# Kernel tuning notes

Hardware: AMD Instinct MI355X
Metric: run time of the kernel (lower is better)

Reference implementation:

```python
import jax, jax.numpy as jnp
import numpy as np

MARGIN = 1.0
N, D, N_CLASSES = 8192, 256, 512


def setup_inputs() -> dict:
    key = jax.random.key(0)
    k1, k2 = jax.random.split(key)
    emb = jax.random.normal(k1, (N, D), dtype=jnp.float32)
    emb = emb / jnp.linalg.norm(emb, axis=1, keepdims=True)  # L2-normalized per docstring
    labels = jax.random.randint(k2, (N,), 0, N_CLASSES, dtype=jnp.int64)
    return {"embeddings": emb, "labels": labels}


def _pairwise_l2(x):
    # torch.cdist(x, x, p=2) via ||a||^2 + ||b||^2 - 2ab, with safe sqrt (zero grad at 0)
    sq = jnp.sum(x * x, axis=1)
    sqd = jnp.maximum(sq[:, None] + sq[None, :] - 2.0 * (x @ x.T), 0.0)
    pos = sqd > 0
    return jnp.where(pos, jnp.sqrt(jnp.where(pos, sqd, 1.0)), 0.0)


def _triplet_loss_semi_hard(embeddings, labels, margin):
    n = embeddings.shape[0]
    dist = _pairwise_l2(embeddings)                      # (N, N)
    labels_eq = labels[None, :] == labels[:, None]       # (N, N)
    labels_neq = ~labels_eq
    eye = jnp.eye(n, dtype=bool)
    pos_mask = labels_eq & ~eye
    valid_anchor = pos_mask.any(axis=1) & labels_neq.any(axis=1)

    NEG_INF = jnp.float32(-jnp.inf)
    POS_INF = jnp.float32(jnp.inf)
    # hardest positive per anchor (max dist among same-label, non-self)
    d_pos = jnp.max(jnp.where(pos_mask, dist, NEG_INF), axis=1)  # (N,)

    neg_dists_only = jnp.where(labels_neq, dist, POS_INF)
    # semi-hard: negatives with d_pos < d < d_pos + margin; fallback to hardest negative
    dp = d_pos[:, None]
    semi_mask = labels_neq & (dist > dp) & (dist < dp + margin)
    has_semi = semi_mask.any(axis=1)
    semi_idx = jnp.argmin(jnp.where(semi_mask, dist, POS_INF), axis=1)
    hard_idx = jnp.argmin(neg_dists_only, axis=1)
    neg_idx = jnp.where(has_semi, semi_idx, hard_idx)

    d_neg = jnp.take_along_axis(dist, neg_idx[:, None], axis=1)[:, 0]  # (N,)
    losses = jax.nn.relu(d_pos - d_neg + margin)
    valid_f = valid_anchor.astype(losses.dtype)
    # mean over valid anchors only (losses[valid_anchor].mean())
    return jnp.sum(losses * valid_f) / jnp.sum(valid_f)


def reference(embeddings, labels):
    return _triplet_loss_semi_hard(embeddings, labels, MARGIN)
```

## Files before the change

### kernel.cpp

```cpp
#include <hip/hip_runtime.h>
#include <hip/hip_bf16.h>
#include <math.h>

#define N 8192
#define D 256
#define MARGIN 1.0f

#define BM 128
#define BN 128
#define NCH 4
#define NB (N / BM)
#define NTRI (NB * (NB + 1) / 2)
#define NCONV (N * D / 4 / 256)
#define NCLS 512
#define CCAP 64
#define RPITCH 257

typedef __attribute__((ext_vector_type(8))) _Float16 half8;
typedef __attribute__((ext_vector_type(4))) _Float16 half4;
typedef __attribute__((ext_vector_type(4))) float f32x4;
typedef unsigned int uint32;
typedef unsigned long long u64;

__global__ __launch_bounds__(256) void k_prep(const float* __restrict__ x,
                                              const int* __restrict__ labels,
                                              _Float16* __restrict__ hp,
                                              float* __restrict__ dpos,
                                              u64* __restrict__ acc_pack,
                                              unsigned* __restrict__ counter) {
    const int b = blockIdx.x;
    const int t = threadIdx.x;

    if (b < NCONV) {
        int i = b * 256 + t;
        float4 v = reinterpret_cast<const float4*>(x)[i];
        half4 h;
        h[0] = (_Float16)v.x; h[1] = (_Float16)v.y;
        h[2] = (_Float16)v.z; h[3] = (_Float16)v.w;
        reinterpret_cast<half4*>(hp)[i] = h;
        if (b == 0 && t == 0) {
            *acc_pack = 0ull;
            *counter = 0u;
        }
        return;
    }

    __shared__ float rows[CCAP * RPITCH];
    __shared__ float sqv[CCAP];
    __shared__ int dpv[CCAP];
    __shared__ int mem[CCAP];
    __shared__ int nmem;

    const int c = b - NCONV;
    if (t == 0) nmem = 0;
    if (t < CCAP) dpv[t] = 0;
    __syncthreads();
    for (int base = 0; base < N; base += 256) {
        int j = base + t;
        if (labels[j] == c) {
            int p = atomicAdd(&nmem, 1);
            if (p < CCAP) mem[p] = j;
        }
    }
    __syncthreads();
    const int M = nmem < CCAP ? nmem : CCAP;

    for (int r = 0; r < M; ++r)
        rows[r * RPITCH + t] = x[(size_t)mem[r] * D + t];
    __syncthreads();

    if (t < M) {
        const float* rp = &rows[t * RPITCH];
        float s = 0.0f;
        for (int d = 0; d < D; ++d) s += rp[d] * rp[d];
        sqv[t] = s;
    }
    __syncthreads();

    for (int p = t; p < M * M; p += 256) {
        int i = p / M, j = p - i * M;
        const float* ri = &rows[i * RPITCH];
        const float* rj = &rows[j * RPITCH];
        float dot = 0.0f;
        for (int d = 0; d < D; ++d) dot = fmaf(ri[d], rj[d], dot);
        float sqd = fmaxf(sqv[i] + sqv[j] - 2.0f * dot, 0.0f);
        if (j != i) atomicMax(&dpv[i], __float_as_int(sqd));
    }
    __syncthreads();
    if (t < M)
        dpos[mem[t]] = (M > 1) ? sqrtf(__int_as_float(dpv[t])) : -1.0f;
}

__global__ __launch_bounds__(512) void k_main(const _Float16* __restrict__ hp,
                                              const int* __restrict__ labels,
                                              const float* __restrict__ dpos,
                                              float* __restrict__ pr_n,
                                              float* __restrict__ pr_s,
                                              float* __restrict__ pc_n,
                                              float* __restrict__ pc_s) {
    __shared__ char Abuf[2][BM * 128];
    __shared__ char Bbuf[2][BN * 128];
    __shared__ float rHi[BM], cHi[BN];
    __shared__ int rlab[BM], clab[BN];
    __shared__ float tmpn[4][BM], tmps[4][BM];

    const int t = threadIdx.x;
    int tb = blockIdx.x;
    int by = (int)((2 * NB + 1 - sqrtf((float)((2 * NB + 1) * (2 * NB + 1)) -
                                       8.0f * (float)tb)) * 0.5f);
    if (by < 0) by = 0;
    if (by > NB - 1) by = NB - 1;
    while (by > 0 && (by * NB - by * (by - 1) / 2) > tb) --by;
    while (((by + 1) * NB - (by + 1) * by / 2) <= tb) ++by;
    const int bx = by + (tb - (by * NB - by * (by - 1) / 2));
    const int r0 = by * BM, c0 = bx * BN;

    const int w = t >> 6, lane = t & 63;
    const int wr = w >> 2, wc = w & 3;

    if (t < BM) {
        rlab[t] = labels[r0 + t];
        float dp = dpos[r0 + t];
        rHi[t] = (2.0f - dp * dp) * 0.5f;
    } else if (t < 256) {
        int u = t - BM;
        clab[u] = labels[c0 + u];
        float dp = dpos[c0 + u];
        cHi[u] = (2.0f - dp * dp) * 0.5f;
    }

    f32x4 acc[4][2] = {};
    f32x4 accT[2][4] = {};

    const int srow = lane >> 3;
    const int scol = ((lane & 7) ^ srow) << 3;
    const _Float16* gA0 = hp + (size_t)(r0 + srow) * D + scol + (size_t)w * 8 * D;
    const _Float16* gB0 = hp + (size_t)(c0 + srow) * D + scol + (size_t)w * 8 * D;
    const int ldso = w * 1024 + lane * 16;

#define STAGE(bufA, bufB, k0e)                                                  \
    {                                                                           \
        _Pragma("unroll")                                                       \
        for (int q = 0; q < 2; ++q) {                                           \
            const _Float16* gpa = gA0 + q * (8 * 8 * D) + (k0e);                \
            const _Float16* gpb = gB0 + q * (8 * 8 * D) + (k0e);                \
            char* lpa = (bufA) + q * 8192 + ldso;                               \
            char* lpb = (bufB) + q * 8192 + ldso;                               \
            __builtin_amdgcn_global_load_lds(                                   \
                (__attribute__((address_space(1))) void*)(void*)gpa,            \
                (__attribute__((address_space(3))) void*)lpa, 16, 0, 0);        \
            __builtin_amdgcn_global_load_lds(                                   \
                (__attribute__((address_space(1))) void*)(void*)gpb,            \
                (__attribute__((address_space(3))) void*)lpb, 16, 0, 0);        \
        }                                                                       \
    }

    STAGE(Abuf[0], Bbuf[0], 0);
    asm volatile("s_waitcnt vmcnt(0)" ::: "memory");
    __syncthreads();

    const int g2 = lane >> 4;
    const int lr = lane & 15;
    const int rsw = lr & 7;

#pragma unroll 1
    for (int s = 0; s < NCH; ++s) {
        const int cur = s & 1;
        if (s < NCH - 1) STAGE(Abuf[cur ^ 1], Bbuf[cur ^ 1], (s + 1) * 64);

#pragma unroll
        for (int kk = 0; kk < 2; ++kk) {
            const int cb = kk * 64 + (g2 << 4);
            half8 aF[4], bF[2];
#pragma unroll
            for (int m = 0; m < 4; ++m) {
                int ra = wr * 64 + m * 16 + lr;
                aF[m] = *reinterpret_cast<const half8*>(
                    Abuf[cur] + ra * 128 + (cb ^ (rsw << 4)));
            }
#pragma unroll
            for (int n = 0; n < 2; ++n) {
                int rb = wc * 32 + n * 16 + lr;
                bF[n] = *reinterpret_cast<const half8*>(
                    Bbuf[cur] + rb * 128 + (cb ^ (rsw << 4)));
            }
#pragma unroll
            for (int m = 0; m < 4; ++m)
#pragma unroll
                for (int n = 0; n < 2; ++n)
                    acc[m][n] = __builtin_amdgcn_mfma_f32_16x16x32_f16(
                        aF[m], bF[n], acc[m][n], 0, 0, 0);
#pragma unroll
            for (int n = 0; n < 2; ++n)
#pragma unroll
                for (int m = 0; m < 4; ++m)
                    accT[n][m] = __builtin_amdgcn_mfma_f32_16x16x32_f16(
                        bF[n], aF[m], accT[n][m], 0, 0, 0);
        }
        __syncthreads();
    }
#undef STAGE

    const float NINF = -__builtin_inff();

    int rowm[4]; int rlm[4]; float rHim[4];
#pragma unroll
    for (int m = 0; m < 4; ++m) {
        rowm[m] = wr * 64 + m * 16 + lr;
        rlm[m] = rlab[rowm[m]];
        rHim[m] = rHi[rowm[m]];
    }
    int4 clA = *reinterpret_cast<const int4*>(&clab[wc * 32 + g2 * 4]);
    int4 clB = *reinterpret_cast<const int4*>(&clab[wc * 32 + 16 + g2 * 4]);
    const int clv[8] = {clA.x, clA.y, clA.z, clA.w, clB.x, clB.y, clB.z, clB.w};
    int coln[2]; int cln[2]; float cHin[2];
#pragma unroll
    for (int n = 0; n < 2; ++n) {
        coln[n] = wc * 32 + n * 16 + lr;
        cln[n] = clab[coln[n]];
        cHin[n] = cHi[coln[n]];
    }
    int rlq[16];
#pragma unroll
    for (int m = 0; m < 4; ++m) {
        int4 rv = *reinterpret_cast<const int4*>(&rlab[wr * 64 + m * 16 + g2 * 4]);
        rlq[m * 4 + 0] = rv.x; rlq[m * 4 + 1] = rv.y;
        rlq[m * 4 + 2] = rv.z; rlq[m * 4 + 3] = rv.w;
    }

#pragma unroll
    for (int m = 0; m < 4; ++m) {
        const int rl = rlm[m];
        const float aHi = rHim[m];
        float an = NINF, ag = NINF;
#pragma unroll
        for (int n = 0; n < 2; ++n)
#pragma unroll
            for (int reg = 0; reg < 4; ++reg) {
                float a = accT[n][m][reg];
                bool neq = (rl != clv[n * 4 + reg]);
                an = fmaxf(an, neq ? a : NINF);
                ag = fmaxf(ag, (neq && a < aHi) ? a : NINF);
            }
        an = fmaxf(an, __shfl_xor(an, 16, 64));
        an = fmaxf(an, __shfl_xor(an, 32, 64));
        ag = fmaxf(ag, __shfl_xor(ag, 16, 64));
        ag = fmaxf(ag, __shfl_xor(ag, 32, 64));
        if (g2 == 0) {
            tmpn[wc][rowm[m]] = an;
            tmps[wc][rowm[m]] = ag;
        }
    }
    __syncthreads();
    if (t < BM) {
        float a0 = fmaxf(tmpn[0][t], tmpn[1][t]);
        float a1 = fmaxf(tmpn[2][t], tmpn[3][t]);
        pr_n[(size_t)tb * BM + t] = fmaxf(a0, a1);
        float b0 = fmaxf(tmps[0][t], tmps[1][t]);
        float b1 = fmaxf(tmps[2][t], tmps[3][t]);
        pr_s[(size_t)tb * BM + t] = fmaxf(b0, b1);
    }
    __syncthreads();

#pragma unroll
    for (int n = 0; n < 2; ++n) {
        const int cl = cln[n];
        const float aHi = cHin[n];
        float an = NINF, ag = NINF;
#pragma unroll
        for (int m = 0; m < 4; ++m)
#pragma unroll
            for (int reg = 0; reg < 4; ++reg) {
                float a = acc[m][n][reg];
                bool neq = (cl != rlq[m * 4 + reg]);
                an = fmaxf(an, neq ? a : NINF);
                ag = fmaxf(ag, (neq && a < aHi) ? a : NINF);
            }
        an = fmaxf(an, __shfl_xor(an, 16, 64));
        an = fmaxf(an, __shfl_xor(an, 32, 64));
        ag = fmaxf(ag, __shfl_xor(ag, 16, 64));
        ag = fmaxf(ag, __shfl_xor(ag, 32, 64));
        if (lane < 16) {
            tmpn[wr][coln[n]] = an;
            tmps[wr][coln[n]] = ag;
        }
    }
    __syncthreads();
    if (t < BN) {
        pc_n[(size_t)tb * BN + t] = fmaxf(tmpn[0][t], tmpn[1][t]);
        pc_s[(size_t)tb * BN + t] = fmaxf(tmps[0][t], tmps[1][t]);
    }
}

__global__ __launch_bounds__(256) void k_finish(const float* __restrict__ dpos,
                                                const float* __restrict__ pr_n,
                                                const float* __restrict__ pr_s,
                                                const float* __restrict__ pc_n,
                                                const float* __restrict__ pc_s,
                                                u64* __restrict__ acc_pack,
                                                unsigned* __restrict__ counter,
                                                float* __restrict__ out) {
    __shared__ float shn[2][128], shs[2][128];
    __shared__ u64 wpart[2];
    const int q = blockIdx.x;
    const int t = threadIdx.x;
    const int half = t >> 7, a = t & 127;
    const int Lr = NB - q;
    const int base = q * NB - q * (q - 1) / 2;
    const int ntiles = Lr + q + 1;
    const float NINF = -__builtin_inff();

    float an = NINF, ag = NINF;
    for (int u = half; u < ntiles; u += 2) {
        size_t off;
        const float *Pn, *Ps;
        if (u < Lr) {
            off = (size_t)(base + u) * BM + a;
            Pn = pr_n; Ps = pr_s;
        } else {
            int byy = u - Lr;
            int tb2 = byy * NB - byy * (byy - 1) / 2 + (q - byy);
            off = (size_t)tb2 * BN + a;
            Pn = pc_n; Ps = pc_s;
        }
        an = fmaxf(an, Pn[off]);
        ag = fmaxf(ag, Ps[off]);
    }
    shn[half][a] = an;
    shs[half][a] = ag;
    __syncthreads();

    u64 pack = 0;
    if (t < 128) {
        an = fmaxf(shn[0][t], shn[1][t]);
        ag = fmaxf(shs[0][t], shs[1][t]);
        float dp = dpos[q * 128 + t];
        if (dp >= 0.0f && an > -1e37f) {
            float dphi = dp + MARGIN;
            float aLo = (2.0f - dphi * dphi) * 0.5f;
            float asel = (ag > aLo) ? ag : an;
            float fsq = fmaxf(fmaf(-2.0f, asel, 2.0f), 0.0f);
            float dn = sqrtf(fsq);
            float l = fmaxf(dp - dn + MARGIN, 0.0f);
            u64 lq = (u64)(l * 1073741824.0f + 0.5f);
            pack = (lq << 16) | 1ull;
        }
    }
    for (int m = 1; m <= 32; m <<= 1) pack += __shfl_xor(pack, m, 64);
    if (t < 128 && (t & 63) == 0) wpart[t >> 6] = pack;
    __syncthreads();
    if (t == 0) {
        atomicAdd(acc_pack, wpart[0] + wpart[1]);
        __threadfence();
        unsigned old = atomicAdd(counter, 1u);
        if (old == gridDim.x - 1) {
            u64 val = atomicAdd(acc_pack, (u64)0);
            double s = (double)(val >> 16) * (1.0 / 1073741824.0);
            double c = (double)(val & 0xFFFFull);
            out[0] = (float)(s / c);
        }
    }
}

extern "C" void kernel_launch(void* const* d_in, const int* in_sizes, int n_in,
                              void* d_out, int out_size, void* d_ws, size_t ws_size,
                              hipStream_t stream) {
    const float* x = (const float*)d_in[0];
    const int* labels = (const int*)d_in[1];
    float* out = (float*)d_out;

    u64* acc_pack = (u64*)d_ws;
    unsigned* counter = (unsigned*)(acc_pack + 1);
    float* dpos = (float*)(counter + 2);
    _Float16* hp = (_Float16*)(dpos + N);
    float* pr_n = (float*)(hp + (size_t)N * D);
    float* pr_s = pr_n + (size_t)NTRI * BM;
    float* pc_n = pr_s + (size_t)NTRI * BM;
    float* pc_s = pc_n + (size_t)NTRI * BM;

    hipLaunchKernelGGL(k_prep, dim3(NCONV + NCLS), dim3(256), 0, stream,
                       x, labels, hp, dpos, acc_pack, counter);
    hipLaunchKernelGGL(k_main, dim3(NTRI), dim3(512), 0, stream,
                       hp, labels, dpos, pr_n, pr_s, pc_n, pc_s);
    hipLaunchKernelGGL(k_finish, dim3(NB), dim3(256), 0, stream,
                       dpos, pr_n, pr_s, pc_n, pc_s, acc_pack, counter, out);
}
```

Before: 97.65 us.

## Fuse finish kernel into main kernel via trailing spin-wait blocks

Removes the separate k_finish launch by appending NB extra blocks to k_main that spin on a done counter until all tile blocks have published their partial maxima, then perform the per-row reduction and loss accumulation. Tile blocks now write partials with agent-scope atomic stores and bump the counter after a fence. This removes one kernel launch and its gap. In exchange, waiting blocks occupy CU slots, which relies on block dispatch order to avoid deadlock, and they use 512 threads where the old finish used 256.

```diff
diff --git a/kernel.cpp b/kernel.cpp
--- a/kernel.cpp
+++ b/kernel.cpp
@@ -27,7 +27,8 @@
                                               _Float16* __restrict__ hp,
                                               float* __restrict__ dpos,
                                               u64* __restrict__ acc_pack,
-                                              unsigned* __restrict__ counter) {
+                                              unsigned* __restrict__ counter,
+                                              unsigned* __restrict__ done_ctr) {
     const int b = blockIdx.x;
     const int t = threadIdx.x;
 
@@ -41,6 +42,7 @@
         if (b == 0 && t == 0) {
             *acc_pack = 0ull;
             *counter = 0u;
+            *done_ctr = 0u;
         }
         return;
     }
@@ -97,14 +99,92 @@
                                               float* __restrict__ pr_n,
                                               float* __restrict__ pr_s,
                                               float* __restrict__ pc_n,
-                                              float* __restrict__ pc_s) {
+                                              float* __restrict__ pc_s,
+                                              u64* __restrict__ acc_pack,
+                                              unsigned* __restrict__ counter,
+                                              unsigned* __restrict__ done_ctr,
+                                              float* __restrict__ out) {
+    const int t = threadIdx.x;
+    const float NINF = -__builtin_inff();
+
+    if (blockIdx.x >= NTRI) {
+        __shared__ float shn[4][128], shs[4][128];
+        __shared__ u64 wpart[2];
+        const int q = blockIdx.x - NTRI;
+        const int part = t >> 7, a = t & 127;
+        const int Lr = NB - q;
+        const int base = q * NB - q * (q - 1) / 2;
+        const int ntiles = Lr + q + 1;
+
+        if (t == 0) {
+            while (__hip_atomic_load(done_ctr, __ATOMIC_RELAXED,
+                                     __HIP_MEMORY_SCOPE_AGENT) < NTRI)
+                __builtin_amdgcn_s_sleep(8);
+        }
+        __syncthreads();
+        __threadfence();
+
+        float an = NINF, ag = NINF;
+        for (int u = part; u < ntiles; u += 4) {
+            size_t off;
+            const float *Pn, *Ps;
+            if (u < Lr) {
+                off = (size_t)(base + u) * BM + a;
+                Pn = pr_n; Ps = pr_s;
+            } else {
+                int byy = u - Lr;
+                int tb2 = byy * NB - byy * (byy - 1) / 2 + (q - byy);
+                off = (size_t)tb2 * BN + a;
+                Pn = pc_n; Ps = pc_s;
+            }
+            an = fmaxf(an, __hip_atomic_load(&Pn[off], __ATOMIC_RELAXED,
+                                             __HIP_MEMORY_SCOPE_AGENT));
+            ag = fmaxf(ag, __hip_atomic_load(&Ps[off], __ATOMIC_RELAXED,
+                                             __HIP_MEMORY_SCOPE_AGENT));
+        }
+        shn[part][a] = an;
+        shs[part][a] = ag;
+        __syncthreads();
+
+        u64 pack = 0;
+        if (t < 128) {
+            an = fmaxf(fmaxf(shn[0][t], shn[1][t]), fmaxf(shn[2][t], shn[3][t]));
+            ag = fmaxf(fmaxf(shs[0][t], shs[1][t]), fmaxf(shs[2][t], shs[3][t]));
+            float dp = dpos[q * 128 + t];
+            if (dp >= 0.0f && an > -1e37f) {
+                float dphi = dp + MARGIN;
+                float aLo = (2.0f - dphi * dphi) * 0.5f;
+                float asel = (ag > aLo) ? ag : an;
+                float fsq = fmaxf(fmaf(-2.0f, asel, 2.0f), 0.0f);
+                float dn = sqrtf(fsq);
+                float l = fmaxf(dp - dn + MARGIN, 0.0f);
+                u64 lq = (u64)(l * 1073741824.0f + 0.5f);
+                pack = (lq << 16) | 1ull;
+            }
+        }
+        for (int m = 1; m <= 32; m <<= 1) pack += __shfl_xor(pack, m, 64);
+        if (t < 128 && (t & 63) == 0) wpart[t >> 6] = pack;
+        __syncthreads();
+        if (t == 0) {
+            atomicAdd(acc_pack, wpart[0] + wpart[1]);
+            __threadfence();
+            unsigned old = atomicAdd(counter, 1u);
+            if (old == NB - 1) {
+                u64 val = atomicAdd(acc_pack, (u64)0);
+                double s = (double)(val >> 16) * (1.0 / 1073741824.0);
+                double c = (double)(val & 0xFFFFull);
+                out[0] = (float)(s / c);
+            }
+        }
+        return;
+    }
+
     __shared__ char Abuf[2][BM * 128];
     __shared__ char Bbuf[2][BN * 128];
     __shared__ float rHi[BM], cHi[BN];
     __shared__ int rlab[BM], clab[BN];
     __shared__ float tmpn[4][BM], tmps[4][BM];
 
-    const int t = threadIdx.x;
     int tb = blockIdx.x;
     int by = (int)((2 * NB + 1 - sqrtf((float)((2 * NB + 1) * (2 * NB + 1)) -
                                        8.0f * (float)tb)) * 0.5f);
@@ -141,11 +221,11 @@
 #define STAGE(bufA, bufB, k0e)                                                  \
     {                                                                           \
         _Pragma("unroll")                                                       \
-        for (int q = 0; q < 2; ++q) {                                           \
-            const _Float16* gpa = gA0 + q * (8 * 8 * D) + (k0e);                \
-            const _Float16* gpb = gB0 + q * (8 * 8 * D) + (k0e);                \
-            char* lpa = (bufA) + q * 8192 + ldso;                               \
-            char* lpb = (bufB) + q * 8192 + ldso;                               \
+        for (int q2 = 0; q2 < 2; ++q2) {                                        \
+            const _Float16* gpa = gA0 + q2 * (8 * 8 * D) + (k0e);               \
+            const _Float16* gpb = gB0 + q2 * (8 * 8 * D) + (k0e);               \
+            char* lpa = (bufA) + q2 * 8192 + ldso;                              \
+            char* lpb = (bufB) + q2 * 8192 + ldso;                              \
             __builtin_amdgcn_global_load_lds(                                   \
                 (__attribute__((address_space(1))) void*)(void*)gpa,            \
                 (__attribute__((address_space(3))) void*)lpa, 16, 0, 0);        \
@@ -201,8 +281,6 @@
     }
 #undef STAGE
 
-    const float NINF = -__builtin_inff();
-
     int rowm[4]; int rlm[4]; float rHim[4];
 #pragma unroll
     for (int m = 0; m < 4; ++m) {
@@ -255,10 +333,12 @@
     if (t < BM) {
         float a0 = fmaxf(tmpn[0][t], tmpn[1][t]);
         float a1 = fmaxf(tmpn[2][t], tmpn[3][t]);
-        pr_n[(size_t)tb * BM + t] = fmaxf(a0, a1);
+        __hip_atomic_store(&pr_n[(size_t)tb * BM + t], fmaxf(a0, a1),
+                           __ATOMIC_RELAXED, __HIP_MEMORY_SCOPE_AGENT);
         float b0 = fmaxf(tmps[0][t], tmps[1][t]);
         float b1 = fmaxf(tmps[2][t], tmps[3][t]);
-        pr_s[(size_t)tb * BM + t] = fmaxf(b0, b1);
+        __hip_atomic_store(&pr_s[(size_t)tb * BM + t], fmaxf(b0, b1),
+                           __ATOMIC_RELAXED, __HIP_MEMORY_SCOPE_AGENT);
     }
     __syncthreads();
 
@@ -287,78 +367,17 @@
     }
     __syncthreads();
     if (t < BN) {
-        pc_n[(size_t)tb * BN + t] = fmaxf(tmpn[0][t], tmpn[1][t]);
-        pc_s[(size_t)tb * BN + t] = fmaxf(tmps[0][t], tmps[1][t]);
-    }
-}
-
-__global__ __launch_bounds__(256) void k_finish(const float* __restrict__ dpos,
-                                                const float* __restrict__ pr_n,
-                                                const float* __restrict__ pr_s,
-                                                const float* __restrict__ pc_n,
-                                                const float* __restrict__ pc_s,
-                                                u64* __restrict__ acc_pack,
-                                                unsigned* __restrict__ counter,
-                                                float* __restrict__ out) {
-    __shared__ float shn[2][128], shs[2][128];
-    __shared__ u64 wpart[2];
-    const int q = blockIdx.x;
-    const int t = threadIdx.x;
-    const int half = t >> 7, a = t & 127;
-    const int Lr = NB - q;
-    const int base = q * NB - q * (q - 1) / 2;
-    const int ntiles = Lr + q + 1;
-    const float NINF = -__builtin_inff();
-
-    float an = NINF, ag = NINF;
-    for (int u = half; u < ntiles; u += 2) {
-        size_t off;
-        const float *Pn, *Ps;
-        if (u < Lr) {
-            off = (size_t)(base + u) * BM + a;
-            Pn = pr_n; Ps = pr_s;
-        } else {
-            int byy = u - Lr;
-            int tb2 = byy * NB - byy * (byy - 1) / 2 + (q - byy);
-            off = (size_t)tb2 * BN + a;
-            Pn = pc_n; Ps = pc_s;
-        }
-        an = fmaxf(an, Pn[off]);
-        ag = fmaxf(ag, Ps[off]);
-    }
-    shn[half][a] = an;
-    shs[half][a] = ag;
-    __syncthreads();
-
-    u64 pack = 0;
-    if (t < 128) {
-        an = fmaxf(shn[0][t], shn[1][t]);
-        ag = fmaxf(shs[0][t], shs[1][t]);
-        float dp = dpos[q * 128 + t];
-        if (dp >= 0.0f && an > -1e37f) {
-            float dphi = dp + MARGIN;
-            float aLo = (2.0f - dphi * dphi) * 0.5f;
-            float asel = (ag > aLo) ? ag : an;
-            float fsq = fmaxf(fmaf(-2.0f, asel, 2.0f), 0.0f);
-            float dn = sqrtf(fsq);
-            float l = fmaxf(dp - dn + MARGIN, 0.0f);
-            u64 lq = (u64)(l * 1073741824.0f + 0.5f);
-            pack = (lq << 16) | 1ull;
-        }
-    }
-    for (int m = 1; m <= 32; m <<= 1) pack += __shfl_xor(pack, m, 64);
-    if (t < 128 && (t & 63) == 0) wpart[t >> 6] = pack;
+        __hip_atomic_store(&pc_n[(size_t)tb * BN + t],
+                           fmaxf(tmpn[0][t], tmpn[1][t]),
+                           __ATOMIC_RELAXED, __HIP_MEMORY_SCOPE_AGENT);
+        __hip_atomic_store(&pc_s[(size_t)tb * BN + t],
+                           fmaxf(tmps[0][t], tmps[1][t]),
+                           __ATOMIC_RELAXED, __HIP_MEMORY_SCOPE_AGENT);
+    }
     __syncthreads();
     if (t == 0) {
-        atomicAdd(acc_pack, wpart[0] + wpart[1]);
         __threadfence();
-        unsigned old = atomicAdd(counter, 1u);
-        if (old == gridDim.x - 1) {
-            u64 val = atomicAdd(acc_pack, (u64)0);
-            double s = (double)(val >> 16) * (1.0 / 1073741824.0);
-            double c = (double)(val & 0xFFFFull);
-            out[0] = (float)(s / c);
-        }
+        atomicAdd(done_ctr, 1u);
     }
 }
 
@@ -371,7 +390,8 @@
 
     u64* acc_pack = (u64*)d_ws;
     unsigned* counter = (unsigned*)(acc_pack + 1);
-    float* dpos = (float*)(counter + 2);
+    unsigned* done_ctr = counter + 1;
+    float* dpos = (float*)(done_ctr + 1);
     _Float16* hp = (_Float16*)(dpos + N);
     float* pr_n = (float*)(hp + (size_t)N * D);
     float* pr_s = pr_n + (size_t)NTRI * BM;
@@ -379,9 +399,8 @@
     float* pc_s = pc_n + (size_t)NTRI * BM;
 
     hipLaunchKernelGGL(k_prep, dim3(NCONV + NCLS), dim3(256), 0, stream,
-                       x, labels, hp, dpos, acc_pack, counter);
-    hipLaunchKernelGGL(k_main, dim3(NTRI), dim3(512), 0, stream,
-                       hp, labels, dpos, pr_n, pr_s, pc_n, pc_s);
-    hipLaunchKernelGGL(k_finish, dim3(NB), dim3(256), 0, stream,
-                       dpos, pr_n, pr_s, pc_n, pc_s, acc_pack, counter, out);
+                       x, labels, hp, dpos, acc_pack, counter, done_ctr);
+    hipLaunchKernelGGL(k_main, dim3(NTRI + NB), dim3(512), 0, stream,
+                       hp, labels, dpos, pr_n, pr_s, pc_n, pc_s,
+                       acc_pack, counter, done_ctr, out);
 }
```

Result: slower. 131.1 us (+34.2%).
